# Kernel tuning notes

Hardware: AMD Instinct MI355X
Metric: run time of the kernel (lower is better)

Reference implementation:

```python
import jax, jax.numpy as jnp
import numpy as np

QMAX = 127.0

def quantize_rowwise(a):
    """bnb-style vector-wise (per-row) absmax int8 quantization.
    Returns (q, scale) with q in [-127, 127] and a ~= q * scale."""
    absmax = jnp.max(jnp.abs(a), axis=-1, keepdims=True)
    scale = jnp.maximum(absmax, 1e-8) / QMAX          # per-row scale
    q = jnp.clip(jnp.round(a / scale), -QMAX, QMAX)   # int8 values (kept float)
    return q, scale

def setup_inputs() -> dict:
    key = jax.random.key(0)
    k1, k2, k3 = jax.random.split(key, 3)
    tokens, d_in, d_out = 8192, 4096, 4096
    x = jax.random.normal(k1, (tokens, d_in), dtype=jnp.float32)
    W = jax.random.normal(k2, (d_out, d_in), dtype=jnp.float32) * 0.02
    bias = jax.random.normal(k3, (d_out,), dtype=jnp.float32) * 0.01
    return {"x": x, "W": W, "bias": bias}

def reference(x, W, bias):
    # Linear8bitLt(has_fp16_weights=False):
    #   weight stored as int8 CB with per-output-channel absmax scale SCB,
    #   input quantized per-row to int8, int8xint8 -> int32 GEMM,
    #   dequant: acc * (scale_x outer scale_w), then + bias.
    qw, sw = quantize_rowwise(W)        # [d_out, d_in], [d_out, 1]
    qx, sx = quantize_rowwise(x)        # [T, d_in],     [T, 1]
    acc = jnp.einsum('ti,oi->to', qx, qw)      # int32 accumulator (emulated in fp32)
    out = acc * (sx * sw.T) + bias[None, :]    # dequantize + bias
    return out
```

## Files before the change

### kernel.cpp

```cpp
#include <hip/hip_runtime.h>

typedef __attribute__((ext_vector_type(4))) int int4v;
typedef __attribute__((ext_vector_type(4))) float float4v;

#define QMAX 127.0f

__global__ __launch_bounds__(256) void quant_rows_kernel(
    const float* __restrict__ a, signed char* __restrict__ q,
    float* __restrict__ scale, int K)
{
    const int row = blockIdx.x;
    const int t = threadIdx.x;
    const float4v* ap = (const float4v*)(a + (size_t)row * K);

    float4v v[4];
#pragma unroll
    for (int i = 0; i < 4; ++i) v[i] = ap[t + 256 * i];

    float m = 0.f;
#pragma unroll
    for (int i = 0; i < 4; ++i) {
        m = fmaxf(m, fabsf(v[i].x));
        m = fmaxf(m, fabsf(v[i].y));
        m = fmaxf(m, fabsf(v[i].z));
        m = fmaxf(m, fabsf(v[i].w));
    }
#pragma unroll
    for (int off = 32; off > 0; off >>= 1)
        m = fmaxf(m, __shfl_down(m, off, 64));
    __shared__ float wmax[4];
    if ((t & 63) == 0) wmax[t >> 6] = m;
    __syncthreads();
    const float am = fmaxf(fmaxf(wmax[0], wmax[1]), fmaxf(wmax[2], wmax[3]));
    const float s = fmaxf(am, 1e-8f) / QMAX;
    if (t == 0) scale[row] = s;

    int* qrow = (int*)(q + (size_t)row * K);
#pragma unroll
    for (int i = 0; i < 4; ++i) {
        int b0 = (int)fminf(fmaxf(rintf(v[i].x / s), -QMAX), QMAX);
        int b1 = (int)fminf(fmaxf(rintf(v[i].y / s), -QMAX), QMAX);
        int b2 = (int)fminf(fmaxf(rintf(v[i].z / s), -QMAX), QMAX);
        int b3 = (int)fminf(fmaxf(rintf(v[i].w / s), -QMAX), QMAX);
        qrow[t + 256 * i] =
            (b0 & 0xff) | ((b1 & 0xff) << 8) | ((b2 & 0xff) << 16) | ((b3 & 0xff) << 24);
    }
}

__global__ __launch_bounds__(256, 2) void gemm_i8_kernel(
    const signed char* __restrict__ qx,
    const signed char* __restrict__ qw,
    const float* __restrict__ sx,
    const float* __restrict__ sw,
    const float* __restrict__ bias,
    float* __restrict__ out,
    int M, int N, int K)
{
    __shared__ signed char smA[128 * 64];
    __shared__ signed char smB[256 * 64];

    const int t = threadIdx.x;
    const int lane = t & 63;
    const int wave = t >> 6;
    const int bm = blockIdx.y, bn = blockIdx.x;
    const int wm = (wave >> 1) * 64;
    const int wn = (wave & 1) * 128;

    int4v acc[4][8];
#pragma unroll
    for (int i = 0; i < 4; ++i)
#pragma unroll
        for (int j = 0; j < 8; ++j)
            acc[i][j] = (int4v)0;

    const int r0 = t >> 2;
    const int c_src = ((t & 3) - ((t >> 3) & 3) + 4) & 3;
    const signed char* gA0 = qx + (size_t)(bm * 128 + r0) * K + c_src * 16;
    const signed char* gA1 = gA0 + (size_t)64 * K;
    const signed char* gB0 = qw + (size_t)(bn * 256 + r0) * K + c_src * 16;
    const signed char* gB1 = gB0 + (size_t)64 * K;
    const signed char* gB2 = gB1 + (size_t)64 * K;
    const signed char* gB3 = gB2 + (size_t)64 * K;
    signed char* lA0 = smA + wave * 1024;
    signed char* lA1 = smA + 4096 + wave * 1024;
    signed char* lB0 = smB + wave * 1024;
    signed char* lB1 = smB + 4096 + wave * 1024;
    signed char* lB2 = smB + 8192 + wave * 1024;
    signed char* lB3 = smB + 12288 + wave * 1024;

    const int l16 = lane & 15;
    const int q = lane >> 4;
    const int cr = (q + ((l16 >> 1) & 3)) & 3;
    const int offA = (wm + l16) * 64 + cr * 16;
    const int offB = (wn + l16) * 64 + cr * 16;

    const int KITER = K >> 6;
    for (int kk = 0; kk < KITER; ++kk) {
        __builtin_amdgcn_global_load_lds((const void*)gA0, (void*)lA0, 16, 0, 0);
        __builtin_amdgcn_global_load_lds((const void*)gA1, (void*)lA1, 16, 0, 0);
        __builtin_amdgcn_global_load_lds((const void*)gB0, (void*)lB0, 16, 0, 0);
        __builtin_amdgcn_global_load_lds((const void*)gB1, (void*)lB1, 16, 0, 0);
        __builtin_amdgcn_global_load_lds((const void*)gB2, (void*)lB2, 16, 0, 0);
        __builtin_amdgcn_global_load_lds((const void*)gB3, (void*)lB3, 16, 0, 0);
        gA0 += 64; gA1 += 64; gB0 += 64; gB1 += 64; gB2 += 64; gB3 += 64;
        __syncthreads();

        int4v aF[4], bF[8];
#pragma unroll
        for (int mi = 0; mi < 4; ++mi)
            aF[mi] = *(const int4v*)(smA + offA + mi * 1024);
#pragma unroll
        for (int ni = 0; ni < 8; ++ni)
            bF[ni] = *(const int4v*)(smB + offB + ni * 1024);
#pragma unroll
        for (int mi = 0; mi < 4; ++mi)
#pragma unroll
            for (int ni = 0; ni < 8; ++ni)
                acc[mi][ni] = __builtin_amdgcn_mfma_i32_16x16x64_i8(
                    aF[mi], bF[ni], acc[mi][ni], 0, 0, 0);
        __syncthreads();
    }

    const int col0 = lane & 15;
    const int row0 = (lane >> 4) * 4;
#pragma unroll
    for (int mi = 0; mi < 4; ++mi) {
#pragma unroll
        for (int r = 0; r < 4; ++r) {
            const int gm = bm * 128 + wm + mi * 16 + row0 + r;
            const float sxr = sx[gm];
            float* orow = out + (size_t)gm * N + bn * 256 + wn;
#pragma unroll
            for (int ni = 0; ni < 8; ++ni) {
                const int gn_local = ni * 16 + col0;
                const int gn = bn * 256 + wn + gn_local;
                orow[gn_local] = (float)acc[mi][ni][r] * (sxr * sw[gn]) + bias[gn];
            }
        }
    }
    (void)M;
}

extern "C" void kernel_launch(void* const* d_in, const int* in_sizes, int n_in,
                              void* d_out, int out_size, void* d_ws, size_t ws_size,
                              hipStream_t stream) {
    const float* x    = (const float*)d_in[0];
    const float* W    = (const float*)d_in[1];
    const float* bias = (const float*)d_in[2];
    float* out = (float*)d_out;

    const int dout = in_sizes[2];
    const int din  = in_sizes[1] / dout;
    const int T    = in_sizes[0] / din;

    signed char* qx = (signed char*)d_ws;
    signed char* qw = qx + (size_t)T * din;
    float* sx = (float*)(qw + (size_t)dout * din);
    float* sw = sx + T;

    quant_rows_kernel<<<T,    256, 0, stream>>>(x, qx, sx, din);
    quant_rows_kernel<<<dout, 256, 0, stream>>>(W, qw, sw, din);

    dim3 grid(dout / 256, T / 128);
    gemm_i8_kernel<<<grid, 256, 0, stream>>>(qx, qw, sx, sw, bias, out, T, dout, din);

    (void)n_in; (void)out_size; (void)ws_size;
}
```

Baseline: 413.6 us.

## Double-buffer LDS in int8 GEMM, swizzle block order, raise occupancy hint

The GEMM main loop now uses two LDS buffers, issuing the next tile's global-to-LDS loads before computing the current one, with explicit vmcnt waits and barriers so memory latency overlaps MFMA work. Workgroup IDs are remapped in an 8-way swizzle to improve L2 reuse of A/B tiles. The launch bound asks for three waves per SIMD instead of two, and quantization replaces per-element division with a double-precision reciprocal multiply. Doubled LDS (48KB) may limit occupancy, and the higher launch bound may force register spills given the 128 int accumulators per thread.

New measurement: 660.5 us. +59.7%, slower.

```diff
diff --git a/kernel.cpp b/kernel.cpp
--- a/kernel.cpp
+++ b/kernel.cpp
@@ -35,19 +35,25 @@
     const float s = fmaxf(am, 1e-8f) / QMAX;
     if (t == 0) scale[row] = s;
 
+    const double inv = 1.0 / (double)s;
+
     int* qrow = (int*)(q + (size_t)row * K);
 #pragma unroll
     for (int i = 0; i < 4; ++i) {
-        int b0 = (int)fminf(fmaxf(rintf(v[i].x / s), -QMAX), QMAX);
-        int b1 = (int)fminf(fmaxf(rintf(v[i].y / s), -QMAX), QMAX);
-        int b2 = (int)fminf(fmaxf(rintf(v[i].z / s), -QMAX), QMAX);
-        int b3 = (int)fminf(fmaxf(rintf(v[i].w / s), -QMAX), QMAX);
+        float r0f = (float)((double)v[i].x * inv);
+        float r1f = (float)((double)v[i].y * inv);
+        float r2f = (float)((double)v[i].z * inv);
+        float r3f = (float)((double)v[i].w * inv);
+        int b0 = (int)fminf(fmaxf(rintf(r0f), -QMAX), QMAX);
+        int b1 = (int)fminf(fmaxf(rintf(r1f), -QMAX), QMAX);
+        int b2 = (int)fminf(fmaxf(rintf(r2f), -QMAX), QMAX);
+        int b3 = (int)fminf(fmaxf(rintf(r3f), -QMAX), QMAX);
         qrow[t + 256 * i] =
             (b0 & 0xff) | ((b1 & 0xff) << 8) | ((b2 & 0xff) << 16) | ((b3 & 0xff) << 24);
     }
 }
 
-__global__ __launch_bounds__(256, 2) void gemm_i8_kernel(
+__global__ __launch_bounds__(256, 3) void gemm_i8_kernel(
     const signed char* __restrict__ qx,
     const signed char* __restrict__ qw,
     const float* __restrict__ sx,
@@ -56,13 +62,21 @@
     float* __restrict__ out,
     int M, int N, int K)
 {
-    __shared__ signed char smA[128 * 64];
-    __shared__ signed char smB[256 * 64];
+    __shared__ signed char smA[2][128 * 64];
+    __shared__ signed char smB[2][256 * 64];
 
     const int t = threadIdx.x;
     const int lane = t & 63;
     const int wave = t >> 6;
-    const int bm = blockIdx.y, bn = blockIdx.x;
+
+    const int nx = gridDim.x;
+    const int nwg = nx * gridDim.y;
+    const int bid = blockIdx.y * nx + blockIdx.x;
+    const int cpx = nwg >> 3;
+    const int swz = (bid & 7) * cpx + (bid >> 3);
+    const int bm = swz / nx;
+    const int bn = swz % nx;
+
     const int wm = (wave >> 1) * 64;
     const int wn = (wave & 1) * 128;
 
@@ -81,45 +95,74 @@
     const signed char* gB1 = gB0 + (size_t)64 * K;
     const signed char* gB2 = gB1 + (size_t)64 * K;
     const signed char* gB3 = gB2 + (size_t)64 * K;
-    signed char* lA0 = smA + wave * 1024;
-    signed char* lA1 = smA + 4096 + wave * 1024;
-    signed char* lB0 = smB + wave * 1024;
-    signed char* lB1 = smB + 4096 + wave * 1024;
-    signed char* lB2 = smB + 8192 + wave * 1024;
-    signed char* lB3 = smB + 12288 + wave * 1024;
+
+    signed char* const lA_0 = smA[0] + wave * 1024;
+    signed char* const lA_1 = smA[1] + wave * 1024;
+    signed char* const lB_0 = smB[0] + wave * 1024;
+    signed char* const lB_1 = smB[1] + wave * 1024;
+
+#define STAGE(b) do {                                                                  \
+        __builtin_amdgcn_global_load_lds((const void*)gA0, (void*)(lA_##b),         16, 0, 0); \
+        __builtin_amdgcn_global_load_lds((const void*)gA1, (void*)(lA_##b + 4096),  16, 0, 0); \
+        __builtin_amdgcn_global_load_lds((const void*)gB0, (void*)(lB_##b),         16, 0, 0); \
+        __builtin_amdgcn_global_load_lds((const void*)gB1, (void*)(lB_##b + 4096),  16, 0, 0); \
+        __builtin_amdgcn_global_load_lds((const void*)gB2, (void*)(lB_##b + 8192),  16, 0, 0); \
+        __builtin_amdgcn_global_load_lds((const void*)gB3, (void*)(lB_##b + 12288), 16, 0, 0); \
+        gA0 += 64; gA1 += 64; gB0 += 64; gB1 += 64; gB2 += 64; gB3 += 64;              \
+    } while (0)
 
     const int l16 = lane & 15;
-    const int q = lane >> 4;
-    const int cr = (q + ((l16 >> 1) & 3)) & 3;
+    const int kq = lane >> 4;
+    const int cr = (kq + ((l16 >> 1) & 3)) & 3;
     const int offA = (wm + l16) * 64 + cr * 16;
     const int offB = (wn + l16) * 64 + cr * 16;
 
+#define COMPUTE(b) do {                                                     \
+        int4v aF[4], bF[8];                                                 \
+        _Pragma("unroll")                                                   \
+        for (int mi = 0; mi < 4; ++mi)                                      \
+            aF[mi] = *(const int4v*)(&smA[b][0] + offA + mi * 1024);        \
+        _Pragma("unroll")                                                   \
+        for (int ni = 0; ni < 8; ++ni)                                      \
+            bF[ni] = *(const int4v*)(&smB[b][0] + offB + ni * 1024);        \
+        _Pragma("unroll")                                                   \
+        for (int mi = 0; mi < 4; ++mi)                                      \
+            _Pragma("unroll")                                               \
+            for (int ni = 0; ni < 8; ++ni)                                  \
+                acc[mi][ni] = __builtin_amdgcn_mfma_i32_16x16x64_i8(        \
+                    aF[mi], bF[ni], acc[mi][ni], 0, 0, 0);                  \
+    } while (0)
+
+#define FENCE() asm volatile("" ::: "memory")
+
     const int KITER = K >> 6;
-    for (int kk = 0; kk < KITER; ++kk) {
-        __builtin_amdgcn_global_load_lds((const void*)gA0, (void*)lA0, 16, 0, 0);
-        __builtin_amdgcn_global_load_lds((const void*)gA1, (void*)lA1, 16, 0, 0);
-        __builtin_amdgcn_global_load_lds((const void*)gB0, (void*)lB0, 16, 0, 0);
-        __builtin_amdgcn_global_load_lds((const void*)gB1, (void*)lB1, 16, 0, 0);
-        __builtin_amdgcn_global_load_lds((const void*)gB2, (void*)lB2, 16, 0, 0);
-        __builtin_amdgcn_global_load_lds((const void*)gB3, (void*)lB3, 16, 0, 0);
-        gA0 += 64; gA1 += 64; gB0 += 64; gB1 += 64; gB2 += 64; gB3 += 64;
-        __syncthreads();
-
-        int4v aF[4], bF[8];
-#pragma unroll
-        for (int mi = 0; mi < 4; ++mi)
-            aF[mi] = *(const int4v*)(smA + offA + mi * 1024);
-#pragma unroll
-        for (int ni = 0; ni < 8; ++ni)
-            bF[ni] = *(const int4v*)(smB + offB + ni * 1024);
-#pragma unroll
-        for (int mi = 0; mi < 4; ++mi)
-#pragma unroll
-            for (int ni = 0; ni < 8; ++ni)
-                acc[mi][ni] = __builtin_amdgcn_mfma_i32_16x16x64_i8(
-                    aF[mi], bF[ni], acc[mi][ni], 0, 0, 0);
-        __syncthreads();
-    }
+
+    STAGE(0);
+    for (int kk = 0; kk < KITER; kk += 2) {
+        STAGE(1);
+        asm volatile("s_waitcnt vmcnt(6)" ::: "memory");
+        __builtin_amdgcn_s_barrier();
+        FENCE();
+        COMPUTE(0);
+        FENCE();
+        __builtin_amdgcn_s_barrier();
+        FENCE();
+        if (kk + 2 < KITER) {
+            STAGE(0);
+            asm volatile("s_waitcnt vmcnt(6)" ::: "memory");
+        } else {
+            asm volatile("s_waitcnt vmcnt(0)" ::: "memory");
+        }
+        __builtin_amdgcn_s_barrier();
+        FENCE();
+        COMPUTE(1);
+        FENCE();
+        __builtin_amdgcn_s_barrier();
+        FENCE();
+    }
+#undef STAGE
+#undef COMPUTE
+#undef FENCE
 
     const int col0 = lane & 15;
     const int row0 = (lane >> 4) * 4;
```
